# Kernel optimization log

Hardware: AMD Instinct MI355X
Metric: run time of the kernel (lower is better)

## Reference

```python
import jax, jax.numpy as jnp
import numpy as np

B = 1
Z, H, W = 8, 48, 180
C = 384
HEADS = 12
WS = (2, 6, 10)  # window size (z, h, w)
N = WS[0] * WS[1] * WS[2]          # 120 tokens per window
NW = (Z // WS[0]) * (H // WS[1]) * (W // WS[2])  # 576 windows
BIAS_ROWS = (2 * WS[2] - 1) * WS[1] * WS[1] * WS[0] * WS[0]  # 2736


def _position_index(ws):
    w0, w1, w2 = ws
    zi = np.arange(w0); zj = -np.arange(w0) * w0
    hi = np.arange(w1); hj = -np.arange(w1) * w1
    ww = np.arange(w2)
    c1 = np.stack(np.meshgrid(zi, hi, ww, indexing='ij')).reshape(3, -1)
    c2 = np.stack(np.meshgrid(zj, hj, ww, indexing='ij')).reshape(3, -1)
    coords = (c1[:, :, None] - c2[:, None, :]).transpose(1, 2, 0).copy()  # (N, N, 3)
    coords[:, :, 2] += w2 - 1
    coords[:, :, 1] *= 2 * w2 - 1
    coords[:, :, 0] *= (2 * w2 - 1) * w1 * w1
    return jnp.asarray(coords.sum(-1).reshape(-1), dtype=jnp.int32)  # (N*N,)

POS_IDX = _position_index(WS)


def setup_inputs() -> dict:
    key = jax.random.key(0)
    ks = jax.random.split(key, 16)
    s = 0.02
    return {
        'x': jax.random.normal(ks[0], (B, Z * H * W, C), dtype=jnp.float32),
        'wqkv': jax.random.normal(ks[1], (C, 3 * C), dtype=jnp.float32) * s,
        'bqkv': jnp.zeros((3 * C,), dtype=jnp.float32),
        'wproj': jax.random.normal(ks[2], (C, C), dtype=jnp.float32) * s,
        'bproj': jnp.zeros((C,), dtype=jnp.float32),
        'bias_table': jax.random.normal(ks[3], (BIAS_ROWS, NW, HEADS), dtype=jnp.float32) * s,
        'g1': jnp.ones((C,), dtype=jnp.float32),
        'b1': jnp.zeros((C,), dtype=jnp.float32),
        'g2': jnp.ones((C,), dtype=jnp.float32),
        'b2': jnp.zeros((C,), dtype=jnp.float32),
        'wm1': jax.random.normal(ks[4], (C, 4 * C), dtype=jnp.float32) * s,
        'bm1': jnp.zeros((4 * C,), dtype=jnp.float32),
        'wm2': jax.random.normal(ks[5], (4 * C, C), dtype=jnp.float32) * s,
        'bm2': jnp.zeros((C,), dtype=jnp.float32),
    }


def _layernorm(x, g, b, eps=1e-5):
    mu = jnp.mean(x, axis=-1, keepdims=True)
    var = jnp.var(x, axis=-1, keepdims=True)
    return (x - mu) * jax.lax.rsqrt(var + eps) * g + b


def _block(x, wqkv, bqkv, wproj, bproj, bias_table, g1, b1, g2, b2, wm1, bm1, wm2, bm2):
    w0, w1, w2 = WS
    d = C // HEADS
    scale = d ** -0.5
    shortcut = x
    xr = x.reshape(B, Z, H, W, C)
    # window_partition -> (B*nW, N, C)
    xw = xr.reshape(B, Z // w0, w0, H // w1, w1, W // w2, w2, C)
    xw = xw.transpose(0, 1, 3, 5, 2, 4, 6, 7).reshape(-1, N, C)
    # qkv projection, split heads: (3, B*nW, heads, N, d)
    qkv = (xw @ wqkv + bqkv).reshape(-1, N, 3, HEADS, d).transpose(2, 0, 3, 1, 4)
    q, k, v = qkv[0], qkv[1], qkv[2]
    attn = jnp.einsum('whnd,whmd->whnm', q * scale, k)  # (B*nW, heads, N, N)
    # earth-specific bias: gather + reshape to (nW, heads, N, N)
    bias = bias_table[POS_IDX].reshape(N, N, NW, HEADS).transpose(2, 3, 0, 1)
    attn = jax.nn.softmax(attn + bias, axis=-1)
    out = jnp.einsum('whnm,whmd->whnd', attn, v)
    # NOTE: source reshapes (B*nW, heads, N, d) -> (B*nW, N, C) directly (no transpose)
    out = out.reshape(-1, N, C)
    out = out @ wproj + bproj
    # window_reverse -> (B, Z*H*W, C)
    xr = out.reshape(B, Z // w0, H // w1, W // w2, w0, w1, w2, C)
    xr = xr.transpose(0, 1, 4, 2, 5, 3, 6, 7).reshape(B, Z * H * W, C)
    x = shortcut + _layernorm(xr, g1, b1)
    # MLP with post-norm residual
    h = jax.nn.gelu(x @ wm1 + bm1, approximate=False)
    m = h @ wm2 + bm2
    return x + _layernorm(m, g2, b2)


def reference(x, wqkv, bqkv, wproj, bproj, bias_table, g1, b1, g2, b2, wm1, bm1, wm2, bm2):
    return _block(x, wqkv, bqkv, wproj, bproj, bias_table, g1, b1, g2, b2, wm1, bm1, wm2, bm2)
```

## Files before the change

### kernel.cpp

```cpp
#include <hip/hip_runtime.h>
#include <math.h>

#define L_TOK 69120
#define C_DIM 384
#define C3 1152
#define C4 1536
#define N_TOK 120
#define N_HEAD 12
#define BIAS_ROWS 2736
#define WH 6912
#define CHUNK 7680
#define NCHUNK 9

typedef __attribute__((ext_vector_type(8))) short short8;
typedef __attribute__((ext_vector_type(4))) float floatx4;

__device__ __forceinline__ unsigned short f2bf(float f) {
    union { float f; unsigned int u; } c; c.f = f;
    unsigned int u = c.u;
    return (unsigned short)((u + 0x7fffu + ((u >> 16) & 1u)) >> 16);
}
__device__ __forceinline__ float bf2f(unsigned short s) {
    union { unsigned int u; float f; } c; c.u = ((unsigned int)s) << 16;
    return c.f;
}

__device__ __forceinline__ void gl_lds16(const void* g, void* l) {
    __builtin_amdgcn_global_load_lds((const __attribute__((address_space(1))) unsigned int*)g,
                                     (__attribute__((address_space(3))) unsigned int*)l, 16, 0, 0);
}

__device__ __forceinline__ int win_to_global(int m) {
    int w_idx = m / N_TOK;
    int n = m - w_idx * N_TOK;
    int zw = w_idx / 144;
    int rem = w_idx - zw * 144;
    int hw = rem / 18;
    int ww = rem - hw * 18;
    int zl = n / 60;
    int r2 = n - zl * 60;
    int hl = r2 / 10;
    int wl = r2 - hl * 10;
    return ((zw * 2 + zl) * 48 + hw * 6 + hl) * 180 + ww * 10 + wl;
}

__global__ __launch_bounds__(256) void k_wt(const float* __restrict__ W,
                                            unsigned short* __restrict__ WT, int K, int N) {
    __shared__ float tle[32][33];
    int n0 = blockIdx.x << 5, k0 = blockIdx.y << 5;
    for (int i = threadIdx.y; i < 32; i += 8)
        tle[i][threadIdx.x] = W[(size_t)(k0 + i) * N + n0 + threadIdx.x];
    __syncthreads();
    for (int i = threadIdx.y; i < 32; i += 8)
        WT[(size_t)(n0 + i) * K + k0 + threadIdx.x] = f2bf(tle[threadIdx.x][i]);
}

__global__ __launch_bounds__(256) void k_bt(const float* __restrict__ Bsrc,
                                            unsigned short* __restrict__ BTt) {
    __shared__ float tle[32][33];
    int c0 = blockIdx.x << 5;
    int r0 = blockIdx.y << 5;
    for (int i = threadIdx.y; i < 32; i += 8) {
        int r = r0 + i;
        if (r < BIAS_ROWS) tle[i][threadIdx.x] = Bsrc[(size_t)r * WH + c0 + threadIdx.x];
    }
    __syncthreads();
    int rr = r0 + threadIdx.x;
    if (rr < BIAS_ROWS)
        for (int i = threadIdx.y; i < 32; i += 8)
            BTt[(size_t)(c0 + i) * BIAS_ROWS + rr] = f2bf(tle[threadIdx.x][i]);
}

template <int K>
__device__ __forceinline__ void mfma_loop(const unsigned short* __restrict__ A,
                                          const unsigned short* __restrict__ BT,
                                          unsigned short* As, unsigned short* Bs,
                                          int m0, int n0, floatx4 acc[4][4]) {
    const int tid = threadIdx.x;
    const int wave = tid >> 6, lane = tid & 63;
    const int wm = (wave >> 1) << 6, wn = (wave & 1) << 6;
    const int lm = lane & 15, lq = lane >> 4;
    const int srow = lane >> 2, scol = (lane & 3) << 3;
    const unsigned short* ags = A + (size_t)(m0 + wave * 32 + srow) * K + scol;
    const unsigned short* bgs = BT + (size_t)(n0 + wave * 32 + srow) * K + scol;
    char* lA = (char*)As + wave * 2048;
    char* lB = (char*)Bs + wave * 2048;
    for (int kk = 0; kk < K; kk += 32) {
        gl_lds16(ags + kk, lA);
        gl_lds16(ags + (size_t)16 * K + kk, lA + 1024);
        gl_lds16(bgs + kk, lB);
        gl_lds16(bgs + (size_t)16 * K + kk, lB + 1024);
        __syncthreads();
        short8 af[4], bq[4];
#pragma unroll
        for (int i = 0; i < 4; ++i) af[i] = *(const short8*)(As + (wm + i * 16 + lm) * 32 + lq * 8);
#pragma unroll
        for (int j = 0; j < 4; ++j) bq[j] = *(const short8*)(Bs + (wn + j * 16 + lm) * 32 + lq * 8);
#pragma unroll
        for (int i = 0; i < 4; ++i)
#pragma unroll
            for (int j = 0; j < 4; ++j)
                acc[i][j] = __builtin_amdgcn_mfma_f32_16x16x32_bf16(af[i], bq[j], acc[i][j], 0, 0, 0);
        __syncthreads();
    }
}

__global__ __launch_bounds__(256) void k_qkv(const float* __restrict__ x,
                                             const unsigned short* __restrict__ wqkvT,
                                             const float* __restrict__ bqkv,
                                             unsigned short* __restrict__ q,
                                             unsigned short* __restrict__ kbuf,
                                             unsigned short* __restrict__ vbuf) {
    __shared__ unsigned short As[128 * 40];
    __shared__ unsigned short Bs[128 * 32];
    const int tid = threadIdx.x;
    const int wave = tid >> 6, lane = tid & 63;
    const int wm = (wave >> 1) << 6, wn = (wave & 1) << 6;
    const int lm = lane & 15, lq = lane >> 4;
    const int m0 = blockIdx.y << 7, n0 = blockIdx.x << 7;
    const int ar = tid >> 1, ah = (tid & 1) << 4;
    const float* xrow = x + (size_t)win_to_global(m0 + ar) * C_DIM + ah;
    unsigned short* aw = As + ar * 40 + ah;
    const int srow = lane >> 2, scol = (lane & 3) << 3;
    const unsigned short* bgs = wqkvT + (size_t)(n0 + wave * 32 + srow) * C_DIM + scol;
    char* lB = (char*)Bs + wave * 2048;

    floatx4 acc[4][4];
#pragma unroll
    for (int i = 0; i < 4; ++i)
#pragma unroll
        for (int j = 0; j < 4; ++j) acc[i][j] = (floatx4){0.f, 0.f, 0.f, 0.f};

    for (int kk = 0; kk < C_DIM; kk += 32) {
        gl_lds16(bgs + kk, lB);
        gl_lds16(bgs + (size_t)16 * C_DIM + kk, lB + 1024);
        float f[16];
        *(float4*)(f) = *(const float4*)(xrow + kk);
        *(float4*)(f + 4) = *(const float4*)(xrow + kk + 4);
        *(float4*)(f + 8) = *(const float4*)(xrow + kk + 8);
        *(float4*)(f + 12) = *(const float4*)(xrow + kk + 12);
        short8 s0, s1;
#pragma unroll
        for (int i = 0; i < 8; ++i) { s0[i] = (short)f2bf(f[i]); s1[i] = (short)f2bf(f[i + 8]); }
        *(short8*)aw = s0;
        *(short8*)(aw + 8) = s1;
        __syncthreads();
        short8 af[4], bq[4];
#pragma unroll
        for (int i = 0; i < 4; ++i) af[i] = *(const short8*)(As + (wm + i * 16 + lm) * 40 + lq * 8);
#pragma unroll
        for (int j = 0; j < 4; ++j) bq[j] = *(const short8*)(Bs + (wn + j * 16 + lm) * 32 + lq * 8);
#pragma unroll
        for (int i = 0; i < 4; ++i)
#pragma unroll
            for (int j = 0; j < 4; ++j)
                acc[i][j] = __builtin_amdgcn_mfma_f32_16x16x32_bf16(af[i], bq[j], acc[i][j], 0, 0, 0);
        __syncthreads();
    }

    const int sel = n0 / C_DIM;
    unsigned short* dst = (sel == 0) ? q : (sel == 1) ? kbuf : vbuf;
    const float scl = (sel == 0) ? 0.17677669529663687f : 1.0f;
#pragma unroll
    for (int i = 0; i < 4; ++i) {
        int rowb = m0 + wm + i * 16 + lq * 4;
        int wi[4], nn[4];
#pragma unroll
        for (int r = 0; r < 4; ++r) {
            int row = rowb + r;
            wi[r] = row / N_TOK;
            nn[r] = row - wi[r] * N_TOK;
        }
#pragma unroll
        for (int j = 0; j < 4; ++j) {
            int colg = n0 + wn + j * 16 + lm;
            float bias = bqkv[colg];
            int c2 = colg - sel * C_DIM;
            int head = c2 >> 5, dd = c2 & 31;
#pragma unroll
            for (int r = 0; r < 4; ++r) {
                unsigned short val = f2bf((acc[i][j][r] + bias) * scl);
                if (sel == 2)
                    dst[((size_t)(wi[r] * N_HEAD + head) * 32 + dd) * N_TOK + nn[r]] = val;
                else
                    dst[(((size_t)(wi[r] * N_HEAD + head) * N_TOK + nn[r]) << 5) + dd] = val;
            }
        }
    }
}

__global__ __launch_bounds__(256) void k_attn(const unsigned short* __restrict__ q,
                                              const unsigned short* __restrict__ k,
                                              const unsigned short* __restrict__ vt,
                                              const unsigned short* __restrict__ btabT,
                                              unsigned short* __restrict__ ao) {
    const int wh = blockIdx.x;
    const int w = wh / N_HEAD;
    const int h = wh - w * N_HEAD;
    __shared__ float blds[BIAS_ROWS];
    __shared__ __align__(16) unsigned short plds[4][16 * 136];
    const int tid = threadIdx.x;
    const unsigned short* bptr = btabT + (size_t)wh * BIAS_ROWS;
    for (int i = tid; i < BIAS_ROWS; i += 256) blds[i] = bf2f(bptr[i]);
    __syncthreads();

    const int wave = tid >> 6, lane = tid & 63;
    const int lm = lane & 15, lq = lane >> 4;
    const unsigned short* kwh = k + (size_t)wh * N_TOK * 32;
    const unsigned short* qwh = q + (size_t)wh * N_TOK * 32;
    const unsigned short* vwh = vt + (size_t)wh * 32 * N_TOK;
    unsigned short* pl = plds[wave];

    short8 kfr[8];
#pragma unroll
    for (int kt = 0; kt < 8; ++kt)
        kfr[kt] = *(const short8*)(kwh + (size_t)(kt * 16 + lm) * 32 + lq * 8);

    int p0v[8], d2v[8], d3v[8];
#pragma unroll
    for (int kt = 0; kt < 8; ++kt) {
        int k0 = kt * 16 + lq * 4;
        int z2 = (k0 >= 60) ? 1 : 0;
        int k0m = k0 - 60 * z2;
        int h2 = k0m / 10;
        int w2 = k0m - 10 * h2;
        p0v[kt] = z2 * 1368 + h2 * 114 - w2;
        d2v[kt] = (w2 == 8) ? 122 : -2;
        d3v[kt] = (w2 == 8) ? 121 : -3;
    }

    for (int qi = 0; qi < 2; ++qi) {
        const int qt = wave + 4 * qi;
        short8 qfr = *(const short8*)(qwh + (size_t)(qt * 16 + lm) * 32 + lq * 8);
        floatx4 sc[8];
#pragma unroll
        for (int kt = 0; kt < 8; ++kt)
            sc[kt] = __builtin_amdgcn_mfma_f32_16x16x32_bf16(kfr[kt], qfr,
                                                             (floatx4){0.f, 0.f, 0.f, 0.f}, 0, 0, 0);
        int qg = qt * 16 + lm;
        int zl = qg / 60;
        int r2 = qg - zl * 60;
        int hl = r2 / 10;
        int wl = r2 - hl * 10;
        int pbase = zl * 684 + hl * 19 + wl + 9;
        pbase = min(pbase, 797);
#pragma unroll
        for (int kt = 0; kt < 8; ++kt) {
            if (kt == 7 && lq >= 2) {
                sc[kt] = (floatx4){-1e30f, -1e30f, -1e30f, -1e30f};
            } else {
                int base = pbase + p0v[kt];
                sc[kt][0] += blds[base];
                sc[kt][1] += blds[base - 1];
                sc[kt][2] += blds[base + d2v[kt]];
                sc[kt][3] += blds[base + d3v[kt]];
            }
        }
        float mx = -1e30f;
#pragma unroll
        for (int kt = 0; kt < 8; ++kt)
#pragma unroll
            for (int r = 0; r < 4; ++r) mx = fmaxf(mx, sc[kt][r]);
        mx = fmaxf(mx, __shfl_xor(mx, 16, 64));
        mx = fmaxf(mx, __shfl_xor(mx, 32, 64));
        float l = 0.f;
#pragma unroll
        for (int kt = 0; kt < 8; ++kt)
#pragma unroll
            for (int r = 0; r < 4; ++r) {
                float p = __expf(sc[kt][r] - mx);
                sc[kt][r] = p;
                l += p;
            }
        l += __shfl_xor(l, 16, 64);
        l += __shfl_xor(l, 32, 64);
        float inv = 1.f / l;
#pragma unroll
        for (int kt = 0; kt < 8; ++kt) {
            uint2 pk;
            pk.x = (unsigned int)f2bf(sc[kt][0] * inv) | ((unsigned int)f2bf(sc[kt][1] * inv) << 16);
            pk.y = (unsigned int)f2bf(sc[kt][2] * inv) | ((unsigned int)f2bf(sc[kt][3] * inv) << 16);
            *(uint2*)(pl + lm * 136 + kt * 16 + lq * 4) = pk;
        }
        floatx4 oac[2] = {(floatx4){0.f, 0.f, 0.f, 0.f}, (floatx4){0.f, 0.f, 0.f, 0.f}};
#pragma unroll
        for (int ks = 0; ks < 4; ++ks) {
            short8 af = *(const short8*)(pl + lm * 136 + ks * 32 + lq * 8);
#pragma unroll
            for (int ct = 0; ct < 2; ++ct) {
                short8 bf = *(const short8*)(vwh + (size_t)(ct * 16 + lm) * N_TOK + ks * 32 + lq * 8);
                oac[ct] = __builtin_amdgcn_mfma_f32_16x16x32_bf16(af, bf, oac[ct], 0, 0, 0);
            }
        }
#pragma unroll
        for (int r = 0; r < 4; ++r) {
            int qg2 = qt * 16 + lq * 4 + r;
            if (qg2 < N_TOK) {
                int rq = qg2 / 12;
                int rr = h * 10 + rq;
                int cc = (qg2 - rq * 12) * 32;
#pragma unroll
                for (int ct = 0; ct < 2; ++ct)
                    ao[((size_t)w * N_TOK + rr) * C_DIM + cc + ct * 16 + lm] = f2bf(oac[ct][r]);
            }
        }
    }
}

__global__ __launch_bounds__(256) void k_proj(const unsigned short* __restrict__ ao,
                                              const unsigned short* __restrict__ wprojT,
                                              const float* __restrict__ bproj,
                                              float* __restrict__ p) {
    __shared__ unsigned short As[128 * 32];
    __shared__ unsigned short Bs[128 * 32];
    const int tid = threadIdx.x;
    const int wave = tid >> 6, lane = tid & 63;
    const int wm = (wave >> 1) << 6, wn = (wave & 1) << 6;
    const int lm = lane & 15, lq = lane >> 4;
    const int m0 = blockIdx.y << 7, n0 = blockIdx.x << 7;
    floatx4 acc[4][4];
#pragma unroll
    for (int i = 0; i < 4; ++i)
#pragma unroll
        for (int j = 0; j < 4; ++j) acc[i][j] = (floatx4){0.f, 0.f, 0.f, 0.f};
    mfma_loop<C_DIM>(ao, wprojT, As, Bs, m0, n0, acc);
#pragma unroll
    for (int i = 0; i < 4; ++i) {
        int rowb = m0 + wm + i * 16 + lq * 4;
        int gg[4];
#pragma unroll
        for (int r = 0; r < 4; ++r) gg[r] = win_to_global(rowb + r);
#pragma unroll
        for (int j = 0; j < 4; ++j) {
            int colg = n0 + wn + j * 16 + lm;
            float bias = bproj[colg];
#pragma unroll
            for (int r = 0; r < 4; ++r)
                p[(size_t)gg[r] * C_DIM + colg] = acc[i][j][r] + bias;
        }
    }
}

__global__ __launch_bounds__(256) void k_mlp1(const unsigned short* __restrict__ x1b,
                                              const unsigned short* __restrict__ wm1T,
                                              const float* __restrict__ bm1,
                                              unsigned short* __restrict__ hbuf) {
    __shared__ unsigned short As[128 * 32];
    __shared__ unsigned short Bs[128 * 32];
    const int tid = threadIdx.x;
    const int wave = tid >> 6, lane = tid & 63;
    const int wm = (wave >> 1) << 6, wn = (wave & 1) << 6;
    const int lm = lane & 15, lq = lane >> 4;
    const int m0 = blockIdx.y << 7, n0 = blockIdx.x << 7;
    floatx4 acc[4][4];
#pragma unroll
    for (int i = 0; i < 4; ++i)
#pragma unroll
        for (int j = 0; j < 4; ++j) acc[i][j] = (floatx4){0.f, 0.f, 0.f, 0.f};
    mfma_loop<C_DIM>(x1b, wm1T, As, Bs, m0, n0, acc);
#pragma unroll
    for (int i = 0; i < 4; ++i) {
        int rowb = m0 + wm + i * 16 + lq * 4;
#pragma unroll
        for (int j = 0; j < 4; ++j) {
            int colg = n0 + wn + j * 16 + lm;
            float bias = bm1[colg];
#pragma unroll
            for (int r = 0; r < 4; ++r) {
                float vv = acc[i][j][r] + bias;
                float ge = 0.5f * vv * (1.f + erff(vv * 0.70710678118654752f));
                hbuf[(size_t)(rowb + r) * C4 + colg] = f2bf(ge);
            }
        }
    }
}

__global__ __launch_bounds__(256) void k_mlp2(const unsigned short* __restrict__ hbuf,
                                              const unsigned short* __restrict__ wm2T,
                                              const float* __restrict__ bm2,
                                              float* __restrict__ mbuf) {
    __shared__ unsigned short As[128 * 32];
    __shared__ unsigned short Bs[128 * 32];
    const int tid = threadIdx.x;
    const int wave = tid >> 6, lane = tid & 63;
    const int wm = (wave >> 1) << 6, wn = (wave & 1) << 6;
    const int lm = lane & 15, lq = lane >> 4;
    const int m0 = blockIdx.y << 7, n0 = blockIdx.x << 7;
    floatx4 acc[4][4];
#pragma unroll
    for (int i = 0; i < 4; ++i)
#pragma unroll
        for (int j = 0; j < 4; ++j) acc[i][j] = (floatx4){0.f, 0.f, 0.f, 0.f};
    mfma_loop<C4>(hbuf, wm2T, As, Bs, m0, n0, acc);
#pragma unroll
    for (int i = 0; i < 4; ++i) {
        int rowb = m0 + wm + i * 16 + lq * 4;
#pragma unroll
        for (int j = 0; j < 4; ++j) {
            int colg = n0 + wn + j * 16 + lm;
            float bias = bm2[colg];
#pragma unroll
            for (int r = 0; r < 4; ++r)
                mbuf[(size_t)(rowb + r) * C_DIM + colg] = acc[i][j][r] + bias;
        }
    }
}

__global__ __launch_bounds__(128) void k_ln_res(const float* __restrict__ src,
                                                const float* __restrict__ resid,
                                                const float* __restrict__ gamma,
                                                const float* __restrict__ beta,
                                                float* __restrict__ outp,
                                                unsigned short* __restrict__ out_bf) {
    const int row = blockIdx.x;
    const int t = threadIdx.x;
    const float* sr = src + (size_t)row * C_DIM;
    float v0 = sr[t], v1 = sr[t + 128], v2 = sr[t + 256];
    __shared__ float rs[128], rq[128];
    rs[t] = v0 + v1 + v2;
    rq[t] = v0 * v0 + v1 * v1 + v2 * v2;
    __syncthreads();
    for (int off = 64; off > 0; off >>= 1) {
        if (t < off) { rs[t] += rs[t + off]; rq[t] += rq[t + off]; }
        __syncthreads();
    }
    float mu = rs[0] * (1.f / 384.f);
    float var = rq[0] * (1.f / 384.f) - mu * mu;
    float rinv = rsqrtf(var + 1e-5f);
    const float* rr = resid + (size_t)row * C_DIM;
    float* orow = outp + (size_t)row * C_DIM;
    float y0 = rr[t]       + (v0 - mu) * rinv * gamma[t]       + beta[t];
    float y1 = rr[t + 128] + (v1 - mu) * rinv * gamma[t + 128] + beta[t + 128];
    float y2 = rr[t + 256] + (v2 - mu) * rinv * gamma[t + 256] + beta[t + 256];
    orow[t] = y0; orow[t + 128] = y1; orow[t + 256] = y2;
    if (out_bf) {
        unsigned short* ob = out_bf + (size_t)row * C_DIM;
        ob[t] = f2bf(y0); ob[t + 128] = f2bf(y1); ob[t + 256] = f2bf(y2);
    }
}

extern "C" void kernel_launch(void* const* d_in, const int* in_sizes, int n_in,
                              void* d_out, int out_size, void* d_ws, size_t ws_size,
                              hipStream_t stream) {
    const float* x     = (const float*)d_in[0];
    const float* wqkv  = (const float*)d_in[1];
    const float* bqkv  = (const float*)d_in[2];
    const float* wproj = (const float*)d_in[3];
    const float* bproj = (const float*)d_in[4];
    const float* btab  = (const float*)d_in[5];
    const float* g1    = (const float*)d_in[6];
    const float* b1    = (const float*)d_in[7];
    const float* g2    = (const float*)d_in[8];
    const float* b2    = (const float*)d_in[9];
    const float* wm1   = (const float*)d_in[10];
    const float* bm1   = (const float*)d_in[11];
    const float* wm2   = (const float*)d_in[12];
    const float* bm2   = (const float*)d_in[13];
    float* outp = (float*)d_out;

    const size_t LC = (size_t)L_TOK * C_DIM;
    if (ws_size < 8 * LC) return;
    char* ws = (char*)d_ws;
    const size_t QB = LC * 2;
    unsigned short* qb  = (unsigned short*)ws;
    unsigned short* kb  = (unsigned short*)(ws + QB);
    unsigned short* vb  = (unsigned short*)(ws + 2 * QB);
    unsigned short* btT = (unsigned short*)(ws + 3 * QB);
    size_t wof = 3 * QB + (size_t)WH * BIAS_ROWS * 2;
    unsigned short* wqkvT = (unsigned short*)(ws + wof);
    unsigned short* wprojT = wqkvT + (size_t)C3 * C_DIM;
    unsigned short* wm1T   = wprojT + (size_t)C_DIM * C_DIM;
    unsigned short* wm2T   = wm1T + (size_t)C_DIM * C4;
    unsigned short* aob = qb;
    float* proj = (float*)(ws + QB);
    float* x1   = proj;
    unsigned short* x1b = qb;
    unsigned short* hbuf = (unsigned short*)(ws + 3 * QB);
    float* mbuf = (float*)(ws + 3 * QB + (size_t)CHUNK * C4 * 2);

    dim3 tb(32, 8);
    k_wt<<<dim3(C3 / 32, C_DIM / 32), tb, 0, stream>>>(wqkv, wqkvT, C_DIM, C3);
    k_wt<<<dim3(C_DIM / 32, C_DIM / 32), tb, 0, stream>>>(wproj, wprojT, C_DIM, C_DIM);
    k_wt<<<dim3(C4 / 32, C_DIM / 32), tb, 0, stream>>>(wm1, wm1T, C_DIM, C4);
    k_wt<<<dim3(C_DIM / 32, C4 / 32), tb, 0, stream>>>(wm2, wm2T, C4, C_DIM);
    k_bt<<<dim3(WH / 32, (BIAS_ROWS + 31) / 32), tb, 0, stream>>>(btab, btT);

    k_qkv<<<dim3(C3 / 128, L_TOK / 128), dim3(256), 0, stream>>>(x, wqkvT, bqkv, qb, kb, vb);
    k_attn<<<dim3(WH), dim3(256), 0, stream>>>(qb, kb, vb, btT, aob);
    k_proj<<<dim3(C_DIM / 128, L_TOK / 128), dim3(256), 0, stream>>>(aob, wprojT, bproj, proj);
    k_ln_res<<<dim3(L_TOK), dim3(128), 0, stream>>>(proj, x, g1, b1, x1, x1b);
    for (int c = 0; c < NCHUNK; ++c) {
        size_t r0 = (size_t)c * CHUNK;
        k_mlp1<<<dim3(C4 / 128, CHUNK / 128), dim3(256), 0, stream>>>(x1b + r0 * C_DIM, wm1T, bm1, hbuf);
        k_mlp2<<<dim3(C_DIM / 128, CHUNK / 128), dim3(256), 0, stream>>>(hbuf, wm2T, bm2, mbuf);
        k_ln_res<<<dim3(CHUNK), dim3(128), 0, stream>>>(mbuf, x1 + r0 * C_DIM, g2, b2, outp + r0 * C_DIM, (unsigned short*)nullptr);
    }
    (void)in_sizes; (void)n_in; (void)out_size;
}
```

Baseline: 1.282 ms.

## Pre-convert x to bf16 for QKV GEMM, enlarge MLP chunks, reuse output buffer

Adds a k_xc kernel that gathers x into window order and converts it to bf16 in the output buffer. The QKV GEMM can then use the shared async global-to-LDS mfma_loop instead of loading fp32 and converting inside the K loop. The MLP chunk size grows from 7680 to 13824 rows (5 chunks instead of 9), giving fewer launches and larger grids. The MLP2 result is written straight into the output and layer-normed in place, which frees workspace for the bigger hidden buffer. The cost is an extra pass over x and a reliance on in-place LayerNorm being safe.

```diff
diff --git a/kernel.cpp b/kernel.cpp
--- a/kernel.cpp
+++ b/kernel.cpp
@@ -9,8 +9,8 @@
 #define N_HEAD 12
 #define BIAS_ROWS 2736
 #define WH 6912
-#define CHUNK 7680
-#define NCHUNK 9
+#define CHUNK 13824
+#define NCHUNK 5
 
 typedef __attribute__((ext_vector_type(8))) short short8;
 typedef __attribute__((ext_vector_type(4))) float floatx4;
@@ -71,6 +71,23 @@
             BTt[(size_t)(c0 + i) * BIAS_ROWS + rr] = f2bf(tle[threadIdx.x][i]);
 }
 
+__global__ __launch_bounds__(256) void k_xc(const float* __restrict__ x,
+                                            unsigned short* __restrict__ xb) {
+    const int m = (blockIdx.x << 2) + (threadIdx.x >> 6);
+    const int lane = threadIdx.x & 63;
+    const float* src = x + (size_t)win_to_global(m) * C_DIM + lane * 6;
+    unsigned short* dst = xb + (size_t)m * C_DIM + lane * 6;
+    float2 a = *(const float2*)(src);
+    float2 b = *(const float2*)(src + 2);
+    float2 c = *(const float2*)(src + 4);
+    unsigned int u0 = (unsigned int)f2bf(a.x) | ((unsigned int)f2bf(a.y) << 16);
+    unsigned int u1 = (unsigned int)f2bf(b.x) | ((unsigned int)f2bf(b.y) << 16);
+    unsigned int u2 = (unsigned int)f2bf(c.x) | ((unsigned int)f2bf(c.y) << 16);
+    *(unsigned int*)(dst) = u0;
+    *(unsigned int*)(dst + 2) = u1;
+    *(unsigned int*)(dst + 4) = u2;
+}
+
 template <int K>
 __device__ __forceinline__ void mfma_loop(const unsigned short* __restrict__ A,
                                           const unsigned short* __restrict__ BT,
@@ -105,58 +122,25 @@
     }
 }
 
-__global__ __launch_bounds__(256) void k_qkv(const float* __restrict__ x,
+__global__ __launch_bounds__(256) void k_qkv(const unsigned short* __restrict__ xb,
                                              const unsigned short* __restrict__ wqkvT,
                                              const float* __restrict__ bqkv,
                                              unsigned short* __restrict__ q,
                                              unsigned short* __restrict__ kbuf,
                                              unsigned short* __restrict__ vbuf) {
-    __shared__ unsigned short As[128 * 40];
+    __shared__ unsigned short As[128 * 32];
     __shared__ unsigned short Bs[128 * 32];
     const int tid = threadIdx.x;
     const int wave = tid >> 6, lane = tid & 63;
     const int wm = (wave >> 1) << 6, wn = (wave & 1) << 6;
     const int lm = lane & 15, lq = lane >> 4;
     const int m0 = blockIdx.y << 7, n0 = blockIdx.x << 7;
-    const int ar = tid >> 1, ah = (tid & 1) << 4;
-    const float* xrow = x + (size_t)win_to_global(m0 + ar) * C_DIM + ah;
-    unsigned short* aw = As + ar * 40 + ah;
-    const int srow = lane >> 2, scol = (lane & 3) << 3;
-    const unsigned short* bgs = wqkvT + (size_t)(n0 + wave * 32 + srow) * C_DIM + scol;
-    char* lB = (char*)Bs + wave * 2048;
-
     floatx4 acc[4][4];
 #pragma unroll
     for (int i = 0; i < 4; ++i)
 #pragma unroll
         for (int j = 0; j < 4; ++j) acc[i][j] = (floatx4){0.f, 0.f, 0.f, 0.f};
-
-    for (int kk = 0; kk < C_DIM; kk += 32) {
-        gl_lds16(bgs + kk, lB);
-        gl_lds16(bgs + (size_t)16 * C_DIM + kk, lB + 1024);
-        float f[16];
-        *(float4*)(f) = *(const float4*)(xrow + kk);
-        *(float4*)(f + 4) = *(const float4*)(xrow + kk + 4);
-        *(float4*)(f + 8) = *(const float4*)(xrow + kk + 8);
-        *(float4*)(f + 12) = *(const float4*)(xrow + kk + 12);
-        short8 s0, s1;
-#pragma unroll
-        for (int i = 0; i < 8; ++i) { s0[i] = (short)f2bf(f[i]); s1[i] = (short)f2bf(f[i + 8]); }
-        *(short8*)aw = s0;
-        *(short8*)(aw + 8) = s1;
-        __syncthreads();
-        short8 af[4], bq[4];
-#pragma unroll
-        for (int i = 0; i < 4; ++i) af[i] = *(const short8*)(As + (wm + i * 16 + lm) * 40 + lq * 8);
-#pragma unroll
-        for (int j = 0; j < 4; ++j) bq[j] = *(const short8*)(Bs + (wn + j * 16 + lm) * 32 + lq * 8);
-#pragma unroll
-        for (int i = 0; i < 4; ++i)
-#pragma unroll
-            for (int j = 0; j < 4; ++j)
-                acc[i][j] = __builtin_amdgcn_mfma_f32_16x16x32_bf16(af[i], bq[j], acc[i][j], 0, 0, 0);
-        __syncthreads();
-    }
+    mfma_loop<C_DIM>(xb, wqkvT, As, Bs, m0, n0, acc);
 
     const int sel = n0 / C_DIM;
     unsigned short* dst = (sel == 0) ? q : (sel == 1) ? kbuf : vbuf;
@@ -466,7 +450,8 @@
     unsigned short* kb  = (unsigned short*)(ws + QB);
     unsigned short* vb  = (unsigned short*)(ws + 2 * QB);
     unsigned short* btT = (unsigned short*)(ws + 3 * QB);
-    size_t wof = 3 * QB + (size_t)WH * BIAS_ROWS * 2;
+    unsigned short* hbuf = (unsigned short*)(ws + 3 * QB);
+    size_t wof = 3 * QB + (size_t)CHUNK * C4 * 2;
     unsigned short* wqkvT = (unsigned short*)(ws + wof);
     unsigned short* wprojT = wqkvT + (size_t)C3 * C_DIM;
     unsigned short* wm1T   = wprojT + (size_t)C_DIM * C_DIM;
@@ -475,8 +460,7 @@
     float* proj = (float*)(ws + QB);
     float* x1   = proj;
     unsigned short* x1b = qb;
-    unsigned short* hbuf = (unsigned short*)(ws + 3 * QB);
-    float* mbuf = (float*)(ws + 3 * QB + (size_t)CHUNK * C4 * 2);
+    unsigned short* xbuf = (unsigned short*)d_out;
 
     dim3 tb(32, 8);
     k_wt<<<dim3(C3 / 32, C_DIM / 32), tb, 0, stream>>>(wqkv, wqkvT, C_DIM, C3);
@@ -485,15 +469,17 @@
     k_wt<<<dim3(C_DIM / 32, C4 / 32), tb, 0, stream>>>(wm2, wm2T, C4, C_DIM);
     k_bt<<<dim3(WH / 32, (BIAS_ROWS + 31) / 32), tb, 0, stream>>>(btab, btT);
 
-    k_qkv<<<dim3(C3 / 128, L_TOK / 128), dim3(256), 0, stream>>>(x, wqkvT, bqkv, qb, kb, vb);
+    k_xc<<<dim3(L_TOK / 4), dim3(256), 0, stream>>>(x, xbuf);
+    k_qkv<<<dim3(C3 / 128, L_TOK / 128), dim3(256), 0, stream>>>(xbuf, wqkvT, bqkv, qb, kb, vb);
     k_attn<<<dim3(WH), dim3(256), 0, stream>>>(qb, kb, vb, btT, aob);
     k_proj<<<dim3(C_DIM / 128, L_TOK / 128), dim3(256), 0, stream>>>(aob, wprojT, bproj, proj);
     k_ln_res<<<dim3(L_TOK), dim3(128), 0, stream>>>(proj, x, g1, b1, x1, x1b);
     for (int c = 0; c < NCHUNK; ++c) {
         size_t r0 = (size_t)c * CHUNK;
+        float* mbuf = outp + r0 * C_DIM;
         k_mlp1<<<dim3(C4 / 128, CHUNK / 128), dim3(256), 0, stream>>>(x1b + r0 * C_DIM, wm1T, bm1, hbuf);
         k_mlp2<<<dim3(C_DIM / 128, CHUNK / 128), dim3(256), 0, stream>>>(hbuf, wm2T, bm2, mbuf);
-        k_ln_res<<<dim3(CHUNK), dim3(128), 0, stream>>>(mbuf, x1 + r0 * C_DIM, g2, b2, outp + r0 * C_DIM, (unsigned short*)nullptr);
+        k_ln_res<<<dim3(CHUNK), dim3(128), 0, stream>>>(mbuf, x1 + r0 * C_DIM, g2, b2, mbuf, (unsigned short*)nullptr);
     }
     (void)in_sizes; (void)n_in; (void)out_size;
 }
```

Result: faster. 1.113 ms (-13.2%).
